# Kernel optimization log

Hardware: AMD Instinct MI355X
Metric: run time of the kernel (lower is better)

## Reference

```python
import jax, jax.numpy as jnp
import numpy as np

B = 32768
HID = 512          # hidden_dim
DIM = 256          # output dim
MAX_N = 17         # max_n + 1
KEY_MID = (MAX_N + HID) // 2   # 264
DEC_MID = (HID + DIM) // 2     # 384
SP_MID = (HID + MAX_N) // 2    # 264


def _linear_params(k, fan_in, fan_out):
    k1, k2 = jax.random.split(k)
    lim = 1.0 / np.sqrt(fan_in)
    W = jax.random.uniform(k1, (fan_in, fan_out), minval=-lim, maxval=lim, dtype=jnp.float32)
    b = jax.random.uniform(k2, (fan_out,), minval=-lim, maxval=lim, dtype=jnp.float32)
    return W, b


def setup_inputs() -> dict:
    key = jax.random.key(0)
    ks = jax.random.split(key, 7)
    z = jax.random.normal(ks[0], (B, HID), dtype=jnp.float32)
    key_W1, key_b1 = _linear_params(ks[1], MAX_N, KEY_MID)
    key_W2, key_b2 = _linear_params(ks[2], KEY_MID, HID)
    dec_W1, dec_b1 = _linear_params(ks[3], HID, DEC_MID)
    dec_W2, dec_b2 = _linear_params(ks[4], DEC_MID, DIM)
    sp_W1, sp_b1 = _linear_params(ks[5], HID, SP_MID)
    sp_W2, sp_b2 = _linear_params(ks[6], SP_MID, MAX_N)
    return dict(
        z=z,
        key_W1=key_W1, key_b1=key_b1,
        key_g1=jnp.ones((KEY_MID,), jnp.float32), key_be1=jnp.zeros((KEY_MID,), jnp.float32),
        key_W2=key_W2, key_b2=key_b2,
        dec_W1=dec_W1, dec_b1=dec_b1, dec_W2=dec_W2, dec_b2=dec_b2,
        sp_W1=sp_W1, sp_b1=sp_b1,
        sp_g1=jnp.ones((SP_MID,), jnp.float32), sp_be1=jnp.zeros((SP_MID,), jnp.float32),
        sp_W2=sp_W2, sp_b2=sp_b2,
    )


def _ln(x, g, b):
    m = x.mean(-1, keepdims=True)
    v = x.var(-1, keepdims=True)
    return (x - m) / jnp.sqrt(v + 1e-5) * g + b


def _ragged_indices(n):
    # n: np.int array [B]; returns batch ids and within-sample positions k
    n = np.asarray(n)
    batch = np.repeat(np.arange(n.shape[0]), n)
    starts = np.concatenate([np.zeros(1, dtype=np.int64), np.cumsum(n)[:-1]])
    k = np.arange(batch.shape[0]) - starts[batch]
    return batch, k


def reference(z, key_W1, key_b1, key_g1, key_be1, key_W2, key_b2,
              dec_W1, dec_b1, dec_W2, dec_b2,
              sp_W1, sp_b1, sp_g1, sp_be1, sp_W2, sp_b2):
    # size_pred MLP: Linear -> LayerNorm -> ReLU -> Linear
    h = jax.nn.relu(_ln(z @ sp_W1 + sp_b1, sp_g1, sp_be1))
    n_pred = h @ sp_W2 + sp_b2                       # [B, MAX_N]
    n = np.asarray(jnp.argmax(n_pred, axis=-1))      # concrete sizes (ragged)
    batch_np, k_np = _ragged_indices(n)
    batch = jnp.asarray(batch_np)
    k = jnp.asarray(k_np)
    pos = jax.nn.one_hot(k, MAX_N, dtype=jnp.float32)            # [T, MAX_N]
    # key_net: Linear -> LayerNorm -> ReLU -> Linear
    keys = jax.nn.relu(_ln(pos @ key_W1 + key_b1, key_g1, key_be1)) @ key_W2 + key_b2  # [T, HID]
    vals_rep = z[batch]                              # repeat_interleave via gather
    zp = vals_rep * keys
    # decoder: Linear -> ReLU -> Linear (no layernorm by default)
    x = jax.nn.relu(zp @ dec_W1 + dec_b1) @ dec_W2 + dec_b2      # [T, DIM]
    return x, batch
```

## Files before the change

### kernel.cpp

```cpp
#include <hip/hip_runtime.h>
#include <hip/hip_bf16.h>

#define B_N   32768
#define HID   512
#define DIM   256
#define MAXN  17
#define SM    264
#define DM    384

typedef __attribute__((ext_vector_type(8))) short bf16x8;
typedef __attribute__((ext_vector_type(4))) float f32x4;

static __device__ __forceinline__ unsigned short f2bf(float x) {
  union { float f; unsigned u; } v; v.f = x;
  unsigned r = (v.u + 0x7FFFu + ((v.u >> 16) & 1u)) >> 16;
  return (unsigned short)r;
}

static __device__ __forceinline__ unsigned pkbf(float a, float b) {
  __hip_bfloat162 h = __float22bfloat162_rn(float2{a, b});
  union { __hip_bfloat162 h; unsigned u; } cv; cv.h = h;
  return cv.u;
}

__global__ __launch_bounds__(320) void sizepred_kernel(
    const float* __restrict__ z,  const float* __restrict__ W1,
    const float* __restrict__ b1, const float* __restrict__ g1,
    const float* __restrict__ be1, const float* __restrict__ W2,
    const float* __restrict__ b2, int* __restrict__ n_out)
{
  __shared__ __align__(16) float us[16 * 268];
  __shared__ float lnm[16], lnr[16];
  __shared__ float log17[16 * 17];

  const int tid = threadIdx.x;
  const int b0  = blockIdx.x * 16;

  const bool act = tid < 264;
  const int  s0  = (tid / 66) * 4;
  const int  j0  = (tid % 66) * 4;

  float acc[4][4];
#pragma unroll
  for (int i = 0; i < 4; ++i)
#pragma unroll
    for (int q = 0; q < 4; ++q) acc[i][q] = 0.f;

  if (act) {
    const float* wp = W1 + j0;
    const float* zp = z + (size_t)(b0 + s0) * 512;
    for (int c0 = 0; c0 < 512; c0 += 8) {
      float a[4][8];
#pragma unroll
      for (int i = 0; i < 4; ++i) {
        float4 lo = *(const float4*)(zp + (size_t)i * 512 + c0);
        float4 hi = *(const float4*)(zp + (size_t)i * 512 + c0 + 4);
        a[i][0] = lo.x; a[i][1] = lo.y; a[i][2] = lo.z; a[i][3] = lo.w;
        a[i][4] = hi.x; a[i][5] = hi.y; a[i][6] = hi.z; a[i][7] = hi.w;
      }
#pragma unroll
      for (int cc = 0; cc < 8; ++cc) {
        float4 bv = *(const float4*)(wp + (size_t)(c0 + cc) * 264);
#pragma unroll
        for (int i = 0; i < 4; ++i) {
          acc[i][0] += a[i][cc] * bv.x;
          acc[i][1] += a[i][cc] * bv.y;
          acc[i][2] += a[i][cc] * bv.z;
          acc[i][3] += a[i][cc] * bv.w;
        }
      }
    }
    float4 bb = *(const float4*)&b1[j0];
#pragma unroll
    for (int i = 0; i < 4; ++i) {
      float4 o;
      o.x = acc[i][0] + bb.x; o.y = acc[i][1] + bb.y;
      o.z = acc[i][2] + bb.z; o.w = acc[i][3] + bb.w;
      *(float4*)&us[(s0 + i) * 268 + j0] = o;
    }
  }
  __syncthreads();

  if (tid < 16) {
    float s = 0.f, q = 0.f;
    for (int j = 0; j < 264; ++j) { float v = us[tid * 268 + j]; s += v; q += v * v; }
    float m   = s / 264.f;
    float var = q / 264.f - m * m;
    lnm[tid] = m;
    lnr[tid] = 1.f / sqrtf(var + 1e-5f);
  }
  __syncthreads();

  for (int idx = tid; idx < 16 * 264; idx += 320) {
    int s = idx / 264, j = idx - s * 264;
    float v = (us[s * 268 + j] - lnm[s]) * lnr[s] * g1[j] + be1[j];
    us[s * 268 + j] = fmaxf(v, 0.f);
  }
  __syncthreads();

  if (tid < 272) {
    int s = tid / 17, jj = tid - s * 17;
    float a = b2[jj];
    const float* up = &us[s * 268];
#pragma unroll 4
    for (int c = 0; c < 264; c += 4) {
      float4 u = *(const float4*)(up + c);
      a += u.x * W2[(c + 0) * 17 + jj];
      a += u.y * W2[(c + 1) * 17 + jj];
      a += u.z * W2[(c + 2) * 17 + jj];
      a += u.w * W2[(c + 3) * 17 + jj];
    }
    log17[tid] = a;
  }
  __syncthreads();

  if (tid < 16) {
    int best = 0; float bv = log17[tid * 17];
    for (int jj = 1; jj < 17; ++jj) {
      float v = log17[tid * 17 + jj];
      if (v > bv) { bv = v; best = jj; }
    }
    n_out[b0 + tid] = best;
  }
}

__global__ __launch_bounds__(1024) void scan_kernel(const int* __restrict__ n,
                                                    int* __restrict__ starts)
{
  __shared__ int part[1024];
  const int tid  = threadIdx.x;
  const int base = tid * 32;
  int loc[32];
  int s = 0;
#pragma unroll
  for (int i = 0; i < 8; ++i) {
    int4 v = ((const int4*)(n + base))[i];
    loc[i * 4 + 0] = v.x; loc[i * 4 + 1] = v.y;
    loc[i * 4 + 2] = v.z; loc[i * 4 + 3] = v.w;
    s += v.x + v.y + v.z + v.w;
  }
  part[tid] = s;
  __syncthreads();
  for (int off = 1; off < 1024; off <<= 1) {
    int v   = part[tid];
    int add = (tid >= off) ? part[tid - off] : 0;
    __syncthreads();
    part[tid] = v + add;
    __syncthreads();
  }
  int run = part[tid] - s;
#pragma unroll
  for (int i = 0; i < 8; ++i) {
    int4 w;
    w.x = run; run += loc[i * 4 + 0];
    w.y = run; run += loc[i * 4 + 1];
    w.z = run; run += loc[i * 4 + 2];
    w.w = run; run += loc[i * 4 + 3];
    ((int4*)(starts + base))[i] = w;
  }
  if (tid == 1023) starts[B_N] = run;
}

__global__ __launch_bounds__(256) void scatter_kernel(
    const int* __restrict__ n, const int* __restrict__ starts,
    int* __restrict__ bi, int* __restrict__ ki, float* __restrict__ out, int T)
{
  int b = blockIdx.x * 256 + threadIdx.x;
  if (b >= B_N) return;
  int st = starts[b], nn = n[b];
  float* ob = out + (size_t)T * DIM;
  for (int k = 0; k < nn; ++k) {
    bi[st + k] = b;
    ki[st + k] = k;
    ob[st + k] = (float)b;
  }
}

__global__ __launch_bounds__(320) void keys_kernel(
    const float* __restrict__ W1, const float* __restrict__ b1,
    const float* __restrict__ g1, const float* __restrict__ be1,
    const float* __restrict__ W2, const float* __restrict__ b2,
    float* __restrict__ ktab)
{
  __shared__ float hs[264];
  __shared__ float mr[2];
  const int kk = blockIdx.x, tid = threadIdx.x;
  if (tid < 264) hs[tid] = W1[kk * 264 + tid] + b1[tid];
  __syncthreads();
  if (tid == 0) {
    float s = 0.f, q = 0.f;
    for (int j = 0; j < 264; ++j) { float v = hs[j]; s += v; q += v * v; }
    float m = s / 264.f;
    mr[0] = m;
    mr[1] = 1.f / sqrtf(q / 264.f - m * m + 1e-5f);
  }
  __syncthreads();
  if (tid < 264) hs[tid] = fmaxf((hs[tid] - mr[0]) * mr[1] * g1[tid] + be1[tid], 0.f);
  __syncthreads();
  for (int c = tid; c < 512; c += 320) {
    float a = b2[c];
    for (int j = 0; j < 264; ++j) a += hs[j] * W2[j * 512 + c];
    ktab[kk * 512 + c] = a;
  }
}

__global__ __launch_bounds__(64) void pack_kernel(
    const float* __restrict__ W1, const float* __restrict__ W2,
    short* __restrict__ W1p, short* __restrict__ W2p)
{
  const int g = blockIdx.x, l = threadIdx.x;
  const float* W; int nt, kt, N;
  if (g < 384) { W = W1; kt = g / 24; nt = g % 24; N = 384; }
  else         { W = W2; int gg = g - 384; kt = gg / 16; nt = gg % 16; N = 256; }
  const int krow = kt * 32 + ((l >> 4) << 3);
  const int col  = nt * 16 + (l & 15);
  short v[8];
#pragma unroll
  for (int j = 0; j < 8; ++j)
    v[j] = (short)f2bf(W[(size_t)(krow + j) * N + col]);
  short* d = (g < 384) ? (W1p + ((size_t)g * 64 + l) * 8)
                       : (W2p + ((size_t)(g - 384) * 64 + l) * 8);
  *(bf16x8*)d = *(bf16x8*)v;
}

__global__ __launch_bounds__(256, 4) void decoder_kernel(
    const float* __restrict__ z,  const float* __restrict__ ktab,
    const short* __restrict__ W1p, const float* __restrict__ b1,
    const short* __restrict__ W2p, const float* __restrict__ b2,
    const int* __restrict__ bi,   const int* __restrict__ ki,
    float* __restrict__ out, int T)
{
  __shared__ __align__(16) short zps[16384];
  __shared__ int tb[32], tk[32];

  const int tid  = threadIdx.x;
  const int wave = tid >> 6;
  const int lane = tid & 63;
  const int t0   = blockIdx.x * 32;

  if (tid < 32) {
    int t = t0 + tid;
    tb[tid] = (t < T) ? bi[t] : 0;
    tk[tid] = (t < T) ? ki[t] : 0;
  }
  __syncthreads();

#pragma unroll
  for (int it = 0; it < 8; ++it) {
    int chunk = tid + it * 256;
    int l  = chunk & 63;
    int mt = (chunk >> 6) & 1;
    int kt = chunk >> 7;
    int m  = mt * 16 + (l & 15);
    int k0 = kt * 32 + ((l >> 4) << 3);
    const float4* zr = (const float4*)(z    + (size_t)tb[m] * 512 + k0);
    const float4* kr = (const float4*)(ktab + (size_t)tk[m] * 512 + k0);
    float4 z0 = zr[0], z1 = zr[1], k4 = kr[0], k5 = kr[1];
    uint4 u;
    u.x = pkbf(z0.x * k4.x, z0.y * k4.y);
    u.y = pkbf(z0.z * k4.z, z0.w * k4.w);
    u.z = pkbf(z1.x * k5.x, z1.y * k5.y);
    u.w = pkbf(z1.z * k5.z, z1.w * k5.w);
    *(uint4*)&zps[(size_t)chunk * 8] = u;
  }
  __syncthreads();

  f32x4 acc[2][6];
#pragma unroll
  for (int mt = 0; mt < 2; ++mt)
#pragma unroll
    for (int j = 0; j < 6; ++j) acc[mt][j] = (f32x4){0.f, 0.f, 0.f, 0.f};

  {
    const short* wb = W1p + ((size_t)(wave * 6) * 64 + lane) * 8;
#pragma unroll 4
    for (int kt = 0; kt < 16; ++kt) {
      bf16x8 a0 = *(bf16x8*)&zps[((kt * 2 + 0) * 64 + lane) * 8];
      bf16x8 a1 = *(bf16x8*)&zps[((kt * 2 + 1) * 64 + lane) * 8];
#pragma unroll
      for (int j = 0; j < 6; ++j) {
        bf16x8 bf = *(const bf16x8*)(wb + (size_t)kt * 12288 + j * 512);
        acc[0][j] = __builtin_amdgcn_mfma_f32_16x16x32_bf16(a0, bf, acc[0][j], 0, 0, 0);
        acc[1][j] = __builtin_amdgcn_mfma_f32_16x16x32_bf16(a1, bf, acc[1][j], 0, 0, 0);
      }
    }
  }
  __syncthreads();

  {
    short* Hs = zps;
    float bload[6];
#pragma unroll
    for (int j = 0; j < 6; ++j)
      bload[j] = b1[wave * 96 + j * 16 + (lane & 15)];
#pragma unroll
    for (int mt = 0; mt < 2; ++mt) {
#pragma unroll
      for (int j = 0; j < 6; ++j) {
        int c = wave * 96 + j * 16 + (lane & 15);
        int lane2hi = ((c >> 3) & 3) << 4;
        int koff = (c >> 5) * 2;
        int jj = c & 7;
        int mbase = mt * 16 + (lane >> 4) * 4;
        int a0 = ((koff + (mbase >> 4)) * 64 + ((mbase & 15) | lane2hi)) * 8 + jj;
        float v0 = fmaxf(acc[mt][j][0] + bload[j], 0.f);
        float v1 = fmaxf(acc[mt][j][1] + bload[j], 0.f);
        float v2 = fmaxf(acc[mt][j][2] + bload[j], 0.f);
        float v3 = fmaxf(acc[mt][j][3] + bload[j], 0.f);
        unsigned p01 = pkbf(v0, v1);
        unsigned p23 = pkbf(v2, v3);
        Hs[a0 +  0] = (short)(p01 & 0xFFFFu);
        Hs[a0 +  8] = (short)(p01 >> 16);
        Hs[a0 + 16] = (short)(p23 & 0xFFFFu);
        Hs[a0 + 24] = (short)(p23 >> 16);
      }
    }
  }
  __syncthreads();

  f32x4 acc2[2][4];
#pragma unroll
  for (int mt = 0; mt < 2; ++mt)
#pragma unroll
    for (int j = 0; j < 4; ++j) acc2[mt][j] = (f32x4){0.f, 0.f, 0.f, 0.f};

  {
    const short* Hs = zps;
    const short* wb = W2p + ((size_t)(wave * 4) * 64 + lane) * 8;
#pragma unroll 4
    for (int kt = 0; kt < 12; ++kt) {
      bf16x8 a0 = *(const bf16x8*)&Hs[((kt * 2 + 0) * 64 + lane) * 8];
      bf16x8 a1 = *(const bf16x8*)&Hs[((kt * 2 + 1) * 64 + lane) * 8];
#pragma unroll
      for (int j = 0; j < 4; ++j) {
        bf16x8 bf = *(const bf16x8*)(wb + (size_t)kt * 8192 + j * 512);
        acc2[0][j] = __builtin_amdgcn_mfma_f32_16x16x32_bf16(a0, bf, acc2[0][j], 0, 0, 0);
        acc2[1][j] = __builtin_amdgcn_mfma_f32_16x16x32_bf16(a1, bf, acc2[1][j], 0, 0, 0);
      }
    }
  }

  {
    float bload[4];
#pragma unroll
    for (int j = 0; j < 4; ++j)
      bload[j] = b2[wave * 64 + j * 16 + (lane & 15)];
#pragma unroll
    for (int mt = 0; mt < 2; ++mt) {
#pragma unroll
      for (int r = 0; r < 4; ++r) {
        int t = t0 + mt * 16 + (lane >> 4) * 4 + r;
        if (t < T) {
#pragma unroll
          for (int j = 0; j < 4; ++j) {
            int c = wave * 64 + j * 16 + (lane & 15);
            out[(size_t)t * 256 + c] = acc2[mt][j][r] + bload[j];
          }
        }
      }
    }
  }
}

extern "C" void kernel_launch(void* const* d_in, const int* in_sizes, int n_in,
                              void* d_out, int out_size, void* d_ws, size_t ws_size,
                              hipStream_t stream)
{
  const float* z      = (const float*)d_in[0];
  const float* keyW1  = (const float*)d_in[1];
  const float* keyb1  = (const float*)d_in[2];
  const float* keyg1  = (const float*)d_in[3];
  const float* keybe1 = (const float*)d_in[4];
  const float* keyW2  = (const float*)d_in[5];
  const float* keyb2  = (const float*)d_in[6];
  const float* decW1  = (const float*)d_in[7];
  const float* decb1  = (const float*)d_in[8];
  const float* decW2  = (const float*)d_in[9];
  const float* decb2  = (const float*)d_in[10];
  const float* spW1   = (const float*)d_in[11];
  const float* spb1   = (const float*)d_in[12];
  const float* spg1   = (const float*)d_in[13];
  const float* spbe1  = (const float*)d_in[14];
  const float* spW2   = (const float*)d_in[15];
  const float* spb2   = (const float*)d_in[16];

  const int T = out_size / (DIM + 1);

  char* ws = (char*)d_ws;
  int*   n_arr  = (int*)(ws);
  int*   starts = (int*)(ws + 131072);
  float* ktab   = (float*)(ws + 262160);
  short* W1p    = (short*)(ws + 296976);
  short* W2p    = (short*)(ws + 690192);
  int*   bi     = (int*)(ws + 886800);
  size_t kioff  = 886800 + (((size_t)T * 4 + 15) / 16) * 16;
  int*   ki     = (int*)(ws + kioff);

  float* outF = (float*)d_out;

  sizepred_kernel<<<B_N / 16, 320, 0, stream>>>(z, spW1, spb1, spg1, spbe1, spW2, spb2, n_arr);
  pack_kernel<<<576, 64, 0, stream>>>(decW1, decW2, W1p, W2p);
  scan_kernel<<<1, 1024, 0, stream>>>(n_arr, starts);
  keys_kernel<<<MAXN, 320, 0, stream>>>(keyW1, keyb1, keyg1, keybe1, keyW2, keyb2, ktab);
  scatter_kernel<<<B_N / 256, 256, 0, stream>>>(n_arr, starts, bi, ki, outF, T);
  if (T > 0)
    decoder_kernel<<<(T + 31) / 32, 256, 0, stream>>>(z, ktab, W1p, decb1, W2p, decb2, bi, ki, outF, T);
}
```

Before: 1.280 ms.

## Stage z tile and double-buffer W1 chunks in LDS for size-pred GEMM

The size-prediction first layer now copies the block's 16 rows of z into shared memory once and streams W1 in 16-row chunks through two shared buffers. Each next chunk is prefetched into registers while the current one is computed. This replaces scattered, repeated global loads of z and W1 with cooperative coalesced loads and LDS reuse. In exchange it needs about 66KB of LDS per block, adds a barrier per chunk, and sets a min-blocks-per-CU hint of 3.

```diff
diff --git a/kernel.cpp b/kernel.cpp
--- a/kernel.cpp
+++ b/kernel.cpp
@@ -23,13 +23,17 @@
   return cv.u;
 }
 
-__global__ __launch_bounds__(320) void sizepred_kernel(
+__global__ __launch_bounds__(320, 3) void sizepred_kernel(
     const float* __restrict__ z,  const float* __restrict__ W1,
     const float* __restrict__ b1, const float* __restrict__ g1,
     const float* __restrict__ be1, const float* __restrict__ W2,
     const float* __restrict__ b2, int* __restrict__ n_out)
 {
-  __shared__ __align__(16) float us[16 * 268];
+  __shared__ __align__(16) char smem[33024 + 2 * 16896];
+  float* zs   = (float*)smem;
+  float* us   = (float*)smem;
+  float* wch0 = (float*)(smem + 33024);
+  float* wch1 = (float*)(smem + 33024 + 16896);
   __shared__ float lnm[16], lnr[16];
   __shared__ float log17[16 * 17];
 
@@ -46,38 +50,85 @@
 #pragma unroll
     for (int q = 0; q < 4; ++q) acc[i][q] = 0.f;
 
+  float4 nz0, nz1, nz2, nz3;
   if (act) {
-    const float* wp = W1 + j0;
-    const float* zp = z + (size_t)(b0 + s0) * 512;
-    for (int c0 = 0; c0 < 512; c0 += 8) {
-      float a[4][8];
-#pragma unroll
-      for (int i = 0; i < 4; ++i) {
-        float4 lo = *(const float4*)(zp + (size_t)i * 512 + c0);
-        float4 hi = *(const float4*)(zp + (size_t)i * 512 + c0 + 4);
-        a[i][0] = lo.x; a[i][1] = lo.y; a[i][2] = lo.z; a[i][3] = lo.w;
-        a[i][4] = hi.x; a[i][5] = hi.y; a[i][6] = hi.z; a[i][7] = hi.w;
-      }
-#pragma unroll
-      for (int cc = 0; cc < 8; ++cc) {
-        float4 bv = *(const float4*)(wp + (size_t)(c0 + cc) * 264);
-#pragma unroll
-        for (int i = 0; i < 4; ++i) {
-          acc[i][0] += a[i][cc] * bv.x;
-          acc[i][1] += a[i][cc] * bv.y;
-          acc[i][2] += a[i][cc] * bv.z;
-          acc[i][3] += a[i][cc] * bv.w;
+    const float4* wsrc = (const float4*)W1;
+    nz0 = wsrc[0 * 264 + tid];
+    nz1 = wsrc[1 * 264 + tid];
+    nz2 = wsrc[2 * 264 + tid];
+    nz3 = wsrc[3 * 264 + tid];
+  }
+  for (int idx = tid; idx < 2048; idx += 320) {
+    int r = idx >> 7, c4 = idx & 127;
+    float4 v = ((const float4*)z)[(size_t)(b0 + r) * 128 + c4];
+    *(float4*)&zs[r * 516 + c4 * 4] = v;
+  }
+  if (act) {
+    float4* wd = (float4*)wch0;
+    wd[0 * 264 + tid] = nz0;
+    wd[1 * 264 + tid] = nz1;
+    wd[2 * 264 + tid] = nz2;
+    wd[3 * 264 + tid] = nz3;
+  }
+  __syncthreads();
+
+#pragma unroll 1
+  for (int ch = 0; ch < 32; ++ch) {
+    const float* cw = (ch & 1) ? wch1 : wch0;
+    float*       nw = (ch & 1) ? wch0 : wch1;
+    if (act && ch + 1 < 32) {
+      const float4* wsrc = (const float4*)(W1 + (size_t)(ch + 1) * 16 * 264);
+      nz0 = wsrc[0 * 264 + tid];
+      nz1 = wsrc[1 * 264 + tid];
+      nz2 = wsrc[2 * 264 + tid];
+      nz3 = wsrc[3 * 264 + tid];
+    }
+    if (act) {
+      const int zb = ch * 16;
+#pragma unroll
+      for (int u = 0; u < 4; ++u) {
+        float4 za0 = *(const float4*)&zs[(s0 + 0) * 516 + zb + u * 4];
+        float4 za1 = *(const float4*)&zs[(s0 + 1) * 516 + zb + u * 4];
+        float4 za2 = *(const float4*)&zs[(s0 + 2) * 516 + zb + u * 4];
+        float4 za3 = *(const float4*)&zs[(s0 + 3) * 516 + zb + u * 4];
+#pragma unroll
+        for (int e = 0; e < 4; ++e) {
+          float4 w = *(const float4*)&cw[(u * 4 + e) * 264 + j0];
+          float a0 = (e == 0) ? za0.x : (e == 1) ? za0.y : (e == 2) ? za0.z : za0.w;
+          float a1 = (e == 0) ? za1.x : (e == 1) ? za1.y : (e == 2) ? za1.z : za1.w;
+          float a2 = (e == 0) ? za2.x : (e == 1) ? za2.y : (e == 2) ? za2.z : za2.w;
+          float a3 = (e == 0) ? za3.x : (e == 1) ? za3.y : (e == 2) ? za3.z : za3.w;
+          acc[0][0] += a0 * w.x; acc[0][1] += a0 * w.y; acc[0][2] += a0 * w.z; acc[0][3] += a0 * w.w;
+          acc[1][0] += a1 * w.x; acc[1][1] += a1 * w.y; acc[1][2] += a1 * w.z; acc[1][3] += a1 * w.w;
+          acc[2][0] += a2 * w.x; acc[2][1] += a2 * w.y; acc[2][2] += a2 * w.z; acc[2][3] += a2 * w.w;
+          acc[3][0] += a3 * w.x; acc[3][1] += a3 * w.y; acc[3][2] += a3 * w.z; acc[3][3] += a3 * w.w;
         }
       }
-    }
+      if (ch + 1 < 32) {
+        float4* wd = (float4*)nw;
+        wd[0 * 264 + tid] = nz0;
+        wd[1 * 264 + tid] = nz1;
+        wd[2 * 264 + tid] = nz2;
+        wd[3 * 264 + tid] = nz3;
+      }
+    }
+    __syncthreads();
+  }
+
+  float4 o0, o1, o2, o3;
+  if (act) {
     float4 bb = *(const float4*)&b1[j0];
-#pragma unroll
-    for (int i = 0; i < 4; ++i) {
-      float4 o;
-      o.x = acc[i][0] + bb.x; o.y = acc[i][1] + bb.y;
-      o.z = acc[i][2] + bb.z; o.w = acc[i][3] + bb.w;
-      *(float4*)&us[(s0 + i) * 268 + j0] = o;
-    }
+    o0.x = acc[0][0] + bb.x; o0.y = acc[0][1] + bb.y; o0.z = acc[0][2] + bb.z; o0.w = acc[0][3] + bb.w;
+    o1.x = acc[1][0] + bb.x; o1.y = acc[1][1] + bb.y; o1.z = acc[1][2] + bb.z; o1.w = acc[1][3] + bb.w;
+    o2.x = acc[2][0] + bb.x; o2.y = acc[2][1] + bb.y; o2.z = acc[2][2] + bb.z; o2.w = acc[2][3] + bb.w;
+    o3.x = acc[3][0] + bb.x; o3.y = acc[3][1] + bb.y; o3.z = acc[3][2] + bb.z; o3.w = acc[3][3] + bb.w;
+  }
+  __syncthreads();
+  if (act) {
+    *(float4*)&us[(s0 + 0) * 268 + j0] = o0;
+    *(float4*)&us[(s0 + 1) * 268 + j0] = o1;
+    *(float4*)&us[(s0 + 2) * 268 + j0] = o2;
+    *(float4*)&us[(s0 + 3) * 268 + j0] = o3;
   }
   __syncthreads();
 
```

New measurement: 1.390 ms. 8.5% more time.
